# Performance work log

Hardware: AMD Instinct MI355X
Metric: run time of the kernel (lower is better)

The kernel has to match this reference:

```python
import jax, jax.numpy as jnp
import numpy as np

N_ENT = 100000
D1 = 200
DA = 30
DS = 30
DO = 20
NUM_SYM = 3
NUM_ASYM = 5
N_REL = 11
BATCH = 1024
REL_PERM = np.array([8, 0, 3, 9, 4, 5, 6, 7, 1, 10, 2], dtype=np.int64)


def build_indices(d1):
    # Replicates the torch index construction exactly (numpy, trace-time constants).
    symu = np.stack([
        np.concatenate([np.zeros(i, np.int64),
                        np.arange((2 * d1 - i + 1) * i // 2, (2 * d1 - i) * (i + 1) // 2, dtype=np.int64)])
        for i in range(d1)])
    syml = np.stack([
        np.concatenate([np.zeros(i + 1, np.int64),
                        np.arange((2 * d1 - i + 1) * i // 2 + 1, (2 * d1 - i) * (i + 1) // 2, dtype=np.int64)])
        for i in range(d1)]).T
    sym_index = symu + syml  # (d1, d1) indices into W1 columns (symmetric layout)
    asym_index = np.stack([
        np.concatenate([np.zeros(i + 1, np.int64),
                        np.arange((2 * d1 - i - 1) * i // 2 + 1, (2 * d1 - i - 2) * (i + 1) // 2 + 1, dtype=np.int64)])
        for i in range(d1)])  # (d1, d1) indices into [0|W2] columns (strict upper layout)
    return sym_index, asym_index


def _batchnorm(x, gamma, beta, eps=1e-5):
    # BatchNorm1d in training mode: biased batch statistics over the batch dim.
    m = jnp.mean(x, axis=0)
    v = jnp.var(x, axis=0)
    return (x - m) * jax.lax.rsqrt(v + eps) * gamma + beta


def setup_inputs() -> dict:
    key = jax.random.key(0)
    ks = jax.random.split(key, 10)
    return {
        "E": 0.1 * jax.random.normal(ks[0], (N_ENT, D1), jnp.float32),
        "R1": 0.1 * jax.random.normal(ks[1], (NUM_SYM, DA), jnp.float32),
        "R2": 0.1 * jax.random.normal(ks[2], (NUM_ASYM, DS), jnp.float32),
        "R3": 0.1 * jax.random.normal(ks[3], (N_REL - NUM_SYM - NUM_ASYM, DA + DS + DO), jnp.float32),
        "W1": jax.random.uniform(ks[4], (DS, D1 * (D1 + 1) // 2), jnp.float32, -1.0, 1.0),
        "W2": jax.random.uniform(ks[5], (DA, D1 * (D1 - 1) // 2), jnp.float32, -1.0, 1.0),
        "W3": jax.random.uniform(ks[6], (DO, D1, D1), jnp.float32, -1.0, 1.0),
        "bn0_gamma": jnp.ones((D1,), jnp.float32),
        "bn0_beta": jnp.zeros((D1,), jnp.float32),
        "bn1_gamma": jnp.ones((D1,), jnp.float32),
        "bn1_beta": jnp.zeros((D1,), jnp.float32),
        "e1_idx": jax.random.randint(ks[7], (BATCH,), 0, N_ENT),
        "r_idx": jax.random.randint(ks[8], (BATCH,), 0, N_REL),
    }


def reference(E, R1, R2, R3, W1, W2, W3, bn0_gamma, bn0_beta, bn1_gamma, bn1_beta, e1_idx, r_idx):
    d1 = E.shape[1]
    sym_index, asym_index = build_indices(d1)

    # construct_RW: relation matrix R (N_REL, ds+da+do) with zero-padded blocks
    R = jnp.concatenate([
        jnp.concatenate([R1, jnp.zeros((NUM_SYM, DA + DO), R1.dtype)], axis=1),
        jnp.concatenate([jnp.zeros((NUM_ASYM, DS), R2.dtype), R2,
                         jnp.zeros((NUM_ASYM, DO), R2.dtype)], axis=1),
        R3,
    ], axis=0)

    # core tensor W (ds+da+do, d1, d1): symmetric slices, antisymmetric slices, free slices
    W2_temp = jnp.concatenate([jnp.zeros((DA, 1), W2.dtype), W2], axis=1)[:, asym_index]
    W = jnp.concatenate([
        W1[:, sym_index],
        W2_temp - jnp.swapaxes(W2_temp, 1, 2),
        W3,
    ], axis=0)

    r = R[jnp.asarray(REL_PERM)[r_idx]]             # (b, K)
    W_mat = jnp.einsum('ijk,bi->bjk', W, r)          # (b, d1, d1)  large intermediate
    x = _batchnorm(E[e1_idx], bn0_gamma, bn0_beta)   # (b, d1)
    x = jnp.einsum('bjk,bj->bk', W_mat, x)           # (b, d1)
    x = _batchnorm(x, bn1_gamma, bn1_beta)
    scores = jnp.einsum('bk,nk->bn', x, E)           # (b, n_ent)
    return jax.nn.sigmoid(scores)
```

## Files before the change

kernel.cpp:

```cpp
#include <hip/hip_runtime.h>
#include <stdint.h>

#define N_ENT 100000
#define D1    200
#define BATCH 1024
#define KPAD  224
#define NPAD  100096
#define NTILES 782

typedef unsigned short ushort_t;
typedef __attribute__((ext_vector_type(8))) short short8;
typedef __attribute__((ext_vector_type(4))) float f32x4;

__constant__ int c_perm[11] = {8, 0, 3, 9, 4, 5, 6, 7, 1, 10, 2};

__device__ __forceinline__ unsigned short f2bf(float f) {
    unsigned int u = __float_as_uint(f);
    unsigned int r = (u + 0x7fffu + ((u >> 16) & 1u)) >> 16;
    return (unsigned short)r;
}

__device__ __forceinline__ int sym_idx(int a, int b) {
    int i = a < b ? a : b;
    int j = a < b ? b : a;
    return i * D1 - (i * (i - 1)) / 2 + (j - i);
}
__device__ __forceinline__ int asym_idx(int i, int j) {
    return i * D1 - (i * (i + 1)) / 2 + (j - i - 1);
}

__global__ void conv_E(const float* __restrict__ E, ushort_t* __restrict__ Epad) {
    int idx = blockIdx.x * 256 + threadIdx.x;
    if (idx >= NPAD * KPAD) return;
    int n = idx / KPAD;
    int k = idx - n * KPAD;
    float v = 0.f;
    if (n < N_ENT && k < D1) v = E[n * D1 + k];
    Epad[idx] = f2bf(v);
}

__global__ void build_M(const float* __restrict__ R1, const float* __restrict__ R2,
                        const float* __restrict__ R3, const float* __restrict__ W1,
                        const float* __restrict__ W2, const float* __restrict__ W3,
                        float* __restrict__ M) {
    int rel = blockIdx.y;
    int e = blockIdx.x * 256 + threadIdx.x;
    if (e >= D1 * D1) return;
    int j = e / D1;
    int k = e - j * D1;
    float acc = 0.f;
    if (rel < 3) {
        int si = sym_idx(j, k);
        #pragma unroll 6
        for (int i = 0; i < 30; i++) acc += R1[rel * 30 + i] * W1[i * 20100 + si];
    } else if (rel < 8) {
        if (j != k) {
            int ai = (j < k) ? asym_idx(j, k) : asym_idx(k, j);
            float s = (j < k) ? 1.f : -1.f;
            #pragma unroll 6
            for (int i = 0; i < 30; i++) acc += R2[(rel - 3) * 30 + i] * s * W2[i * 19900 + ai];
        }
    } else {
        const float* r3 = R3 + (rel - 8) * 80;
        int si = sym_idx(j, k);
        #pragma unroll 6
        for (int i = 0; i < 30; i++) acc += r3[i] * W1[i * 20100 + si];
        if (j != k) {
            int ai = (j < k) ? asym_idx(j, k) : asym_idx(k, j);
            float s = (j < k) ? 1.f : -1.f;
            #pragma unroll 6
            for (int i = 0; i < 30; i++) acc += r3[30 + i] * s * W2[i * 19900 + ai];
        }
        #pragma unroll 5
        for (int i = 0; i < 20; i++) acc += r3[60 + i] * W3[i * 40000 + e];
    }
    M[rel * 40000 + e] = acc;
}

__global__ void bn0_stats(const float* __restrict__ E, const int* __restrict__ e1_idx,
                          const float* __restrict__ gamma, const float* __restrict__ beta,
                          float* __restrict__ scale, float* __restrict__ shift) {
    int f = blockIdx.x;
    int tid = threadIdx.x;
    float s = 0.f, sq = 0.f;
    for (int b = tid; b < BATCH; b += 256) {
        float v = E[e1_idx[b] * D1 + f];
        s += v; sq += v * v;
    }
    __shared__ float ls[256], lq[256];
    ls[tid] = s; lq[tid] = sq;
    __syncthreads();
    for (int off = 128; off > 0; off >>= 1) {
        if (tid < off) { ls[tid] += ls[tid + off]; lq[tid] += lq[tid + off]; }
        __syncthreads();
    }
    if (tid == 0) {
        float m = ls[0] * (1.f / BATCH);
        float var = lq[0] * (1.f / BATCH) - m * m;
        float rstd = rsqrtf(var + 1e-5f);
        scale[f] = rstd * gamma[f];
        shift[f] = beta[f] - m * rstd * gamma[f];
    }
}

__global__ void bn1_stats(const float* __restrict__ y,
                          const float* __restrict__ gamma, const float* __restrict__ beta,
                          float* __restrict__ scale, float* __restrict__ shift) {
    int f = blockIdx.x;
    int tid = threadIdx.x;
    float s = 0.f, sq = 0.f;
    for (int b = tid; b < BATCH; b += 256) {
        float v = y[b * D1 + f];
        s += v; sq += v * v;
    }
    __shared__ float ls[256], lq[256];
    ls[tid] = s; lq[tid] = sq;
    __syncthreads();
    for (int off = 128; off > 0; off >>= 1) {
        if (tid < off) { ls[tid] += ls[tid + off]; lq[tid] += lq[tid + off]; }
        __syncthreads();
    }
    if (tid == 0) {
        float m = ls[0] * (1.f / BATCH);
        float var = lq[0] * (1.f / BATCH) - m * m;
        float rstd = rsqrtf(var + 1e-5f);
        scale[f] = rstd * gamma[f];
        shift[f] = beta[f] - m * rstd * gamma[f];
    }
}

__global__ void xw_kernel(const float* __restrict__ E, const int* __restrict__ e1_idx,
                          const int* __restrict__ r_idx,
                          const float* __restrict__ scale0, const float* __restrict__ shift0,
                          const float* __restrict__ M, float* __restrict__ y) {
    int b = blockIdx.x;
    int tid = threadIdx.x;
    __shared__ float xs[D1];
    __shared__ int s_rel;
    if (tid == 0) s_rel = c_perm[r_idx[b]];
    int e1 = e1_idx[b];
    if (tid < D1) xs[tid] = E[e1 * D1 + tid] * scale0[tid] + shift0[tid];
    __syncthreads();
    if (tid < D1) {
        const float* Mr = M + s_rel * 40000;
        float acc = 0.f;
        #pragma unroll 8
        for (int j = 0; j < D1; j++) acc += xs[j] * Mr[j * D1 + tid];
        y[b * D1 + tid] = acc;
    }
}

__global__ void x2pad_kernel(const float* __restrict__ y,
                             const float* __restrict__ scale1, const float* __restrict__ shift1,
                             ushort_t* __restrict__ x2) {
    int idx = blockIdx.x * 256 + threadIdx.x;
    if (idx >= BATCH * KPAD) return;
    int b = idx / KPAD;
    int k = idx - b * KPAD;
    float v = 0.f;
    if (k < D1) v = y[b * D1 + k] * scale1[k] + shift1[k];
    x2[idx] = f2bf(v);
}

__device__ __forceinline__ void gld_lds16(const void* g, void* l) {
    __builtin_amdgcn_global_load_lds(
        (const __attribute__((address_space(1))) unsigned int*)(uintptr_t)g,
        (__attribute__((address_space(3))) unsigned int*)(unsigned int)(uintptr_t)l,
        16, 0, 0);
}

__global__ __launch_bounds__(256) void gemm_score(const ushort_t* __restrict__ x2,
                                                  const ushort_t* __restrict__ Epad,
                                                  float* __restrict__ out) {
    __shared__ ushort_t As[128 * 32];
    __shared__ ushort_t Bs[128 * 32];
    const int tid = threadIdx.x;
    const int wave = tid >> 6;
    const int lane = tid & 63;
    const int wm = wave >> 1, wn = wave & 1;
    const int quad = lane >> 4, l16 = lane & 15;
    const int tile_n = blockIdx.x * 128;
    const int tile_m = blockIdx.y * 128;

    const int srow = tid >> 2;
    const int sseg = tid & 3;

    f32x4 acc[4][4];
    #pragma unroll
    for (int i = 0; i < 4; i++)
        #pragma unroll
        for (int j = 0; j < 4; j++) acc[i][j] = (f32x4){0.f, 0.f, 0.f, 0.f};

    for (int kb = 0; kb < KPAD; kb += 32) {
        #pragma unroll
        for (int rr = 0; rr < 2; rr++) {
            const ushort_t* ga = x2 + (tile_m + rr * 64 + srow) * KPAD + kb + sseg * 8;
            gld_lds16(ga, &As[rr * 2048 + wave * 512]);
            const ushort_t* gb = Epad + (tile_n + rr * 64 + srow) * KPAD + kb + sseg * 8;
            gld_lds16(gb, &Bs[rr * 2048 + wave * 512]);
        }
        __syncthreads();

        short8 a_frag[4], b_frag[4];
        #pragma unroll
        for (int f = 0; f < 4; f++) {
            a_frag[f] = *(const short8*)&As[(wm * 64 + f * 16 + l16) * 32 + quad * 8];
            b_frag[f] = *(const short8*)&Bs[(wn * 64 + f * 16 + l16) * 32 + quad * 8];
        }
        #pragma unroll
        for (int fm = 0; fm < 4; fm++)
            #pragma unroll
            for (int fn = 0; fn < 4; fn++)
                acc[fm][fn] = __builtin_amdgcn_mfma_f32_16x16x32_bf16(
                    a_frag[fm], b_frag[fn], acc[fm][fn], 0, 0, 0);
        __syncthreads();
    }

    #pragma unroll
    for (int fm = 0; fm < 4; fm++) {
        int m = tile_m + wm * 64 + fm * 16 + quad * 4;
        #pragma unroll
        for (int fn = 0; fn < 4; fn++) {
            int n = tile_n + wn * 64 + fn * 16 + l16;
            if (n < N_ENT) {
                float* po = out + (size_t)m * N_ENT + n;
                #pragma unroll
                for (int r = 0; r < 4; r++) {
                    float v = acc[fm][fn][r];
                    po[(size_t)r * N_ENT] = 1.f / (1.f + __expf(-v));
                }
            }
        }
    }
}

extern "C" void kernel_launch(void* const* d_in, const int* in_sizes, int n_in,
                              void* d_out, int out_size, void* d_ws, size_t ws_size,
                              hipStream_t stream) {
    const float* E  = (const float*)d_in[0];
    const float* R1 = (const float*)d_in[1];
    const float* R2 = (const float*)d_in[2];
    const float* R3 = (const float*)d_in[3];
    const float* W1 = (const float*)d_in[4];
    const float* W2 = (const float*)d_in[5];
    const float* W3 = (const float*)d_in[6];
    const float* g0 = (const float*)d_in[7];
    const float* b0 = (const float*)d_in[8];
    const float* g1 = (const float*)d_in[9];
    const float* b1 = (const float*)d_in[10];
    const int* e1_idx = (const int*)d_in[11];
    const int* r_idx  = (const int*)d_in[12];
    float* out = (float*)d_out;

    char* ws = (char*)d_ws;
    ushort_t* Epad = (ushort_t*)ws;
    float* M       = (float*)(ws + 44843008);
    float* scale0  = (float*)(ws + 46603008);
    float* shift0  = scale0 + D1;
    float* scale1  = shift0 + D1;
    float* shift1  = scale1 + D1;
    float* y       = shift1 + D1;
    ushort_t* x2   = (ushort_t*)(y + BATCH * D1);

    conv_E<<<(NPAD * KPAD + 255) / 256, 256, 0, stream>>>(E, Epad);
    build_M<<<dim3((D1 * D1 + 255) / 256, 11), 256, 0, stream>>>(R1, R2, R3, W1, W2, W3, M);
    bn0_stats<<<D1, 256, 0, stream>>>(E, e1_idx, g0, b0, scale0, shift0);
    xw_kernel<<<BATCH, 256, 0, stream>>>(E, e1_idx, r_idx, scale0, shift0, M, y);
    bn1_stats<<<D1, 256, 0, stream>>>(y, g1, b1, scale1, shift1);
    x2pad_kernel<<<(BATCH * KPAD + 255) / 256, 256, 0, stream>>>(y, scale1, shift1, x2);
    gemm_score<<<dim3(NTILES, BATCH / 128), 256, 0, stream>>>(x2, Epad, out);
}
```

Measured before the change: 632.8 us.

## Vectorize conversion kernels, double-buffer GEMM LDS loads, swap grid order

The E and x2 conversion kernels now handle 8 elements per thread, using 16-byte vector loads and stores instead of scalar ones. The score GEMM gains double-buffered LDS tiles: the next K-slice is issued before computing the current one, with explicit vmcnt waits and barriers. The grid is also transposed so consecutive blocks share the same E tile across the M tiles, which should improve L2 reuse of Epad. The costs are double the LDS use and hand-placed waitcnt logic that relies on the count of outstanding loads.

```diff
diff --git a/kernel.cpp b/kernel.cpp
--- a/kernel.cpp
+++ b/kernel.cpp
@@ -31,12 +31,22 @@
 
 __global__ void conv_E(const float* __restrict__ E, ushort_t* __restrict__ Epad) {
     int idx = blockIdx.x * 256 + threadIdx.x;
-    if (idx >= NPAD * KPAD) return;
-    int n = idx / KPAD;
-    int k = idx - n * KPAD;
-    float v = 0.f;
-    if (n < N_ENT && k < D1) v = E[n * D1 + k];
-    Epad[idx] = f2bf(v);
+    if (idx >= NPAD * KPAD / 8) return;
+    int n = idx / (KPAD / 8);
+    int k0 = (idx - n * (KPAD / 8)) * 8;
+    short8 o;
+    if (n < N_ENT && k0 < D1) {
+        const float* src = E + n * D1 + k0;
+        f32x4 v0 = *(const f32x4*)src;
+        f32x4 v1 = *(const f32x4*)(src + 4);
+        o[0] = (short)f2bf(v0[0]); o[1] = (short)f2bf(v0[1]);
+        o[2] = (short)f2bf(v0[2]); o[3] = (short)f2bf(v0[3]);
+        o[4] = (short)f2bf(v1[0]); o[5] = (short)f2bf(v1[1]);
+        o[6] = (short)f2bf(v1[2]); o[7] = (short)f2bf(v1[3]);
+    } else {
+        o = (short8){0, 0, 0, 0, 0, 0, 0, 0};
+    }
+    *(short8*)&Epad[idx * 8] = o;
 }
 
 __global__ void build_M(const float* __restrict__ R1, const float* __restrict__ R2,
@@ -154,12 +164,23 @@
                              const float* __restrict__ scale1, const float* __restrict__ shift1,
                              ushort_t* __restrict__ x2) {
     int idx = blockIdx.x * 256 + threadIdx.x;
-    if (idx >= BATCH * KPAD) return;
-    int b = idx / KPAD;
-    int k = idx - b * KPAD;
-    float v = 0.f;
-    if (k < D1) v = y[b * D1 + k] * scale1[k] + shift1[k];
-    x2[idx] = f2bf(v);
+    if (idx >= BATCH * KPAD / 8) return;
+    int b = idx / (KPAD / 8);
+    int k0 = (idx - b * (KPAD / 8)) * 8;
+    short8 o;
+    if (k0 < D1) {
+        const float* src = y + b * D1 + k0;
+        f32x4 v0 = *(const f32x4*)src;
+        f32x4 v1 = *(const f32x4*)(src + 4);
+        #pragma unroll
+        for (int j = 0; j < 4; j++) {
+            o[j]     = (short)f2bf(v0[j] * scale1[k0 + j]     + shift1[k0 + j]);
+            o[j + 4] = (short)f2bf(v1[j] * scale1[k0 + j + 4] + shift1[k0 + j + 4]);
+        }
+    } else {
+        o = (short8){0, 0, 0, 0, 0, 0, 0, 0};
+    }
+    *(short8*)&x2[idx * 8] = o;
 }
 
 __device__ __forceinline__ void gld_lds16(const void* g, void* l) {
@@ -172,18 +193,21 @@
 __global__ __launch_bounds__(256) void gemm_score(const ushort_t* __restrict__ x2,
                                                   const ushort_t* __restrict__ Epad,
                                                   float* __restrict__ out) {
-    __shared__ ushort_t As[128 * 32];
-    __shared__ ushort_t Bs[128 * 32];
+    __shared__ ushort_t As[2][128 * 32];
+    __shared__ ushort_t Bs[2][128 * 32];
     const int tid = threadIdx.x;
     const int wave = tid >> 6;
     const int lane = tid & 63;
     const int wm = wave >> 1, wn = wave & 1;
     const int quad = lane >> 4, l16 = lane & 15;
-    const int tile_n = blockIdx.x * 128;
-    const int tile_m = blockIdx.y * 128;
+    const int tile_m = blockIdx.x * 128;
+    const int tile_n = blockIdx.y * 128;
 
     const int srow = tid >> 2;
     const int sseg = tid & 3;
+
+    const ushort_t* gA = x2 + (tile_m + srow) * KPAD + sseg * 8;
+    const ushort_t* gB = Epad + (size_t)(tile_n + srow) * KPAD + sseg * 8;
 
     f32x4 acc[4][4];
     #pragma unroll
@@ -191,21 +215,32 @@
         #pragma unroll
         for (int j = 0; j < 4; j++) acc[i][j] = (f32x4){0.f, 0.f, 0.f, 0.f};
 
-    for (int kb = 0; kb < KPAD; kb += 32) {
-        #pragma unroll
-        for (int rr = 0; rr < 2; rr++) {
-            const ushort_t* ga = x2 + (tile_m + rr * 64 + srow) * KPAD + kb + sseg * 8;
-            gld_lds16(ga, &As[rr * 2048 + wave * 512]);
-            const ushort_t* gb = Epad + (tile_n + rr * 64 + srow) * KPAD + kb + sseg * 8;
-            gld_lds16(gb, &Bs[rr * 2048 + wave * 512]);
-        }
-        __syncthreads();
+#define STAGE(c, kb) do {                                                     \
+        gld_lds16(gA + (kb),              &As[c][wave * 512]);                \
+        gld_lds16(gA + 64 * KPAD + (kb),  &As[c][2048 + wave * 512]);         \
+        gld_lds16(gB + (kb),              &Bs[c][wave * 512]);                \
+        gld_lds16(gB + 64 * KPAD + (kb),  &Bs[c][2048 + wave * 512]);         \
+    } while (0)
+
+    STAGE(0, 0);
+
+    #pragma unroll
+    for (int t = 0; t < KPAD / 32; ++t) {
+        const int cur = t & 1;
+        if (t < KPAD / 32 - 1) {
+            STAGE(cur ^ 1, (t + 1) * 32);
+            asm volatile("s_waitcnt vmcnt(4)" ::: "memory");
+        } else {
+            asm volatile("s_waitcnt vmcnt(0)" ::: "memory");
+        }
+        __builtin_amdgcn_s_barrier();
+        __builtin_amdgcn_sched_barrier(0);
 
         short8 a_frag[4], b_frag[4];
         #pragma unroll
         for (int f = 0; f < 4; f++) {
-            a_frag[f] = *(const short8*)&As[(wm * 64 + f * 16 + l16) * 32 + quad * 8];
-            b_frag[f] = *(const short8*)&Bs[(wn * 64 + f * 16 + l16) * 32 + quad * 8];
+            a_frag[f] = *(const short8*)&As[cur][(wm * 64 + f * 16 + l16) * 32 + quad * 8];
+            b_frag[f] = *(const short8*)&Bs[cur][(wn * 64 + f * 16 + l16) * 32 + quad * 8];
         }
         #pragma unroll
         for (int fm = 0; fm < 4; fm++)
@@ -213,8 +248,11 @@
             for (int fn = 0; fn < 4; fn++)
                 acc[fm][fn] = __builtin_amdgcn_mfma_f32_16x16x32_bf16(
                     a_frag[fm], b_frag[fn], acc[fm][fn], 0, 0, 0);
-        __syncthreads();
-    }
+
+        __builtin_amdgcn_s_barrier();
+        __builtin_amdgcn_sched_barrier(0);
+    }
+#undef STAGE
 
     #pragma unroll
     for (int fm = 0; fm < 4; fm++) {
@@ -262,11 +300,11 @@
     float* y       = shift1 + D1;
     ushort_t* x2   = (ushort_t*)(y + BATCH * D1);
 
-    conv_E<<<(NPAD * KPAD + 255) / 256, 256, 0, stream>>>(E, Epad);
+    conv_E<<<(NPAD * KPAD / 8 + 255) / 256, 256, 0, stream>>>(E, Epad);
     build_M<<<dim3((D1 * D1 + 255) / 256, 11), 256, 0, stream>>>(R1, R2, R3, W1, W2, W3, M);
     bn0_stats<<<D1, 256, 0, stream>>>(E, e1_idx, g0, b0, scale0, shift0);
     xw_kernel<<<BATCH, 256, 0, stream>>>(E, e1_idx, r_idx, scale0, shift0, M, y);
     bn1_stats<<<D1, 256, 0, stream>>>(y, g1, b1, scale1, shift1);
-    x2pad_kernel<<<(BATCH * KPAD + 255) / 256, 256, 0, stream>>>(y, scale1, shift1, x2);
-    gemm_score<<<dim3(NTILES, BATCH / 128), 256, 0, stream>>>(x2, Epad, out);
-}
+    x2pad_kernel<<<(BATCH * KPAD / 8 + 255) / 256, 256, 0, stream>>>(y, scale1, shift1, x2);
+    gemm_score<<<dim3(BATCH / 128, NTILES), 256, 0, stream>>>(x2, Epad, out);
+}
```

Measured after the change: 654.7 us. 1.03x slower.
